# Kernel tuning notes

Hardware: AMD Instinct MI355X
Metric: run time of the kernel (lower is better)

Reference implementation:

```python
import jax, jax.numpy as jnp
import numpy as np

D_MODEL = 1024
NUM_HEADS = 16


def setup_inputs() -> dict:
    key = jax.random.key(0)
    ks = jax.random.split(key, 5)
    std = float(np.sqrt(2.0 / (D_MODEL + D_MODEL)))
    def w(k):
        # approximate trunc_normal init with clipped normal (init only; math of fwd unaffected)
        v = jax.random.truncated_normal(k, -3.0, 3.0, (D_MODEL, D_MODEL), jnp.float32) * std
        return v
    x = jax.random.normal(ks[0], (4, 2048, D_MODEL), jnp.float32)
    return {
        "x": x,
        "wq": w(ks[1]),
        "wk": w(ks[2]),
        "wv": w(ks[3]),
        "wo": w(ks[4]),
    }


def reference(x, wq, wk, wv, wo):
    b, s, d = x.shape
    h = NUM_HEADS
    dk = d // h
    # Linear: einsum('o i, ... i -> ... o')
    def proj(w):
        y = jnp.einsum('oi,bsi->bso', w, x)
        return y.reshape(b, s, h, dk).transpose(0, 2, 1, 3)  # b h s dk
    Q, K, V = proj(wq), proj(wk), proj(wv)
    scale = 1.0 / jnp.sqrt(jnp.asarray(dk, x.dtype))
    scores = jnp.einsum('bhqd,bhkd->bhqk', Q, K) * scale
    mask = jnp.tril(jnp.ones((s, s), dtype=bool))
    scores = jnp.where(mask, scores, -jnp.inf)
    attn = jax.nn.softmax(scores, axis=-1)
    out = jnp.einsum('bhqk,bhkd->bhqd', attn, V)
    out = out.transpose(0, 2, 1, 3).reshape(b, s, d)
    return jnp.einsum('oi,bsi->bso', wo, out)
```

## Files before the change

kernel.cpp:

```cpp
#include <hip/hip_runtime.h>
#include <hip/hip_bf16.h>


typedef __bf16 bf16x8 __attribute__((ext_vector_type(8)));
typedef __bf16 bf16x4 __attribute__((ext_vector_type(4)));
typedef float  f32x4  __attribute__((ext_vector_type(4)));
typedef float  f32x16 __attribute__((ext_vector_type(16)));
typedef unsigned int u32x4_t __attribute__((ext_vector_type(4)));

#define GLOBAL_AS __attribute__((address_space(1)))
#define LDS_AS    __attribute__((address_space(3)))

__device__ __forceinline__ void gload16(const void* g, void* l) {
    __builtin_amdgcn_global_load_lds((const GLOBAL_AS void*)g, (LDS_AS void*)l, 16, 0, 0);
}

__device__ __forceinline__ unsigned int cvtpk_bf16(float lo, float hi) {
    unsigned int r;
    asm("v_cvt_pk_bf16_f32 %0, %1, %2" : "=v"(r) : "v"(lo), "v"(hi));
    return r;
}

#define WAITVM0 asm volatile("s_waitcnt vmcnt(0)" ::: "memory")
#define SCHEDB  __builtin_amdgcn_sched_barrier(0)

__global__ __launch_bounds__(256) void cast_kernel(
    const float* __restrict__ x, const float* __restrict__ wq,
    const float* __restrict__ wk, const float* __restrict__ wv,
    const float* __restrict__ wo, __bf16* __restrict__ xb, __bf16* __restrict__ wb) {
    int bid = blockIdx.x;
    const float* src; __bf16* dst; int base;
    if (bid < 4096) {
        src = x; dst = xb; base = bid * 2048;
    } else {
        int r = bid - 4096; int wi = r >> 9;
        src = (wi == 0) ? wq : (wi == 1) ? wk : (wi == 2) ? wv : wo;
        dst = wb + wi * 1048576; base = (r & 511) * 2048;
    }
    int idx = base + threadIdx.x * 8;
    float4 a = *(const float4*)(src + idx);
    float4 b = *(const float4*)(src + idx + 4);
    bf16x8 o;
    o[0] = (__bf16)a.x; o[1] = (__bf16)a.y; o[2] = (__bf16)a.z; o[3] = (__bf16)a.w;
    o[4] = (__bf16)b.x; o[5] = (__bf16)b.y; o[6] = (__bf16)b.z; o[7] = (__bf16)b.w;
    *(bf16x8*)(dst + idx) = o;
}

__global__ __launch_bounds__(256) void gemm_qkv_kernel(
    const __bf16* __restrict__ A, const __bf16* __restrict__ W,
    __bf16* __restrict__ Qb, __bf16* __restrict__ Kb, __bf16* __restrict__ Vt,
    float qscale) {
    __shared__ __align__(16) char lds[65536];
    const int t = threadIdx.x;
    const int wid = t >> 6, lane = t & 63;
    const int g = lane >> 4, m = lane & 15;
    const int wm = wid >> 1, wn = wid & 1;
    const int bid = (blockIdx.x & 7) * 192 + (blockIdx.x >> 3);
    const int mt = bid / 24, nt = bid % 24;
    const int m0 = mt * 128, n0 = nt * 128;
    const bool isV = (n0 >= 2048);

    const __bf16* sA[4]; const __bf16* sB[4]; int dA[4];
#pragma unroll
    for (int i = 0; i < 4; ++i) {
        const int ci = i * 256 + t;
        const int row = ci >> 3;
        const int k8 = (ci & 7) ^ (row & 7);
        sA[i] = A + (size_t)(m0 + row) * 1024 + k8 * 8;
        sB[i] = W + (size_t)(n0 + row) * 1024 + k8 * 8;
        dA[i] = ci * 16;
    }
    auto stage = [&](int kt, char* buf) {
#pragma unroll
        for (int i = 0; i < 4; ++i) gload16(sA[i] + kt * 64, buf + dA[i]);
#pragma unroll
        for (int i = 0; i < 4; ++i) gload16(sB[i] + kt * 64, buf + 16384 + dA[i]);
    };

    const int sw = (m & 7) << 4;
    const int offA = (wm * 64 + m) * 128 + ((g << 4) ^ sw);
    const int offB = (wn * 64 + m) * 128 + ((g << 4) ^ sw);

    stage(0, lds);

    f32x4 acc[4][4] = {};
    for (int kt = 0; kt < 16; ++kt) {
        char* cbuf = lds + (kt & 1) * 32768;
        WAITVM0;
        SCHEDB;
        __builtin_amdgcn_s_barrier();
        SCHEDB;
        if (kt < 15) stage(kt + 1, lds + ((kt + 1) & 1) * 32768);
        const char* bA = cbuf;
        const char* bB = cbuf + 16384;
        bf16x8 a0[4], b0[4], a1[4], b1[4];
#pragma unroll
        for (int i = 0; i < 4; ++i) {
            a0[i] = *(const bf16x8*)(bA + (offA + i * 2048));
            b0[i] = *(const bf16x8*)(bB + (offB + i * 2048));
            a1[i] = *(const bf16x8*)(bA + ((offA + i * 2048) ^ 64));
            b1[i] = *(const bf16x8*)(bB + ((offB + i * 2048) ^ 64));
        }
        __builtin_amdgcn_s_setprio(1);
        if (isV) {
#pragma unroll
            for (int mi = 0; mi < 4; ++mi)
#pragma unroll
                for (int ni = 0; ni < 4; ++ni)
                    acc[mi][ni] = __builtin_amdgcn_mfma_f32_16x16x32_bf16(a0[mi], b0[ni], acc[mi][ni], 0, 0, 0);
#pragma unroll
            for (int mi = 0; mi < 4; ++mi)
#pragma unroll
                for (int ni = 0; ni < 4; ++ni)
                    acc[mi][ni] = __builtin_amdgcn_mfma_f32_16x16x32_bf16(a1[mi], b1[ni], acc[mi][ni], 0, 0, 0);
        } else {
#pragma unroll
            for (int mi = 0; mi < 4; ++mi)
#pragma unroll
                for (int ni = 0; ni < 4; ++ni)
                    acc[mi][ni] = __builtin_amdgcn_mfma_f32_16x16x32_bf16(b0[ni], a0[mi], acc[mi][ni], 0, 0, 0);
#pragma unroll
            for (int mi = 0; mi < 4; ++mi)
#pragma unroll
                for (int ni = 0; ni < 4; ++ni)
                    acc[mi][ni] = __builtin_amdgcn_mfma_f32_16x16x32_bf16(b1[ni], a1[mi], acc[mi][ni], 0, 0, 0);
        }
        __builtin_amdgcn_s_setprio(0);
    }

    if (isV) {
        const int bb = m0 >> 11;
        const int sb = (m0 & 2047) + wm * 64 + 4 * g;
        const int hbase = ((n0 - 2048) >> 6) + wn;
#pragma unroll
        for (int mi = 0; mi < 4; ++mi)
#pragma unroll
            for (int ni = 0; ni < 4; ++ni) {
                const int d = ni * 16 + m;
                bf16x4 pk;
                pk[0] = (__bf16)(acc[mi][ni][0]); pk[1] = (__bf16)(acc[mi][ni][1]);
                pk[2] = (__bf16)(acc[mi][ni][2]); pk[3] = (__bf16)(acc[mi][ni][3]);
                *(bf16x4*)(Vt + ((size_t)(bb * 16 + hbase) * 64 + d) * 2048 + sb + mi * 16) = pk;
            }
    } else {
        __bf16* C = (n0 < 1024) ? Qb : Kb;
        const float sc = (n0 < 1024) ? qscale : 1.f;
        const int cb = (n0 & 1023) + wn * 64 + 4 * g;
        const int row = m0 + wm * 64 + m;
#pragma unroll
        for (int mi = 0; mi < 4; ++mi)
#pragma unroll
            for (int ni = 0; ni < 4; ++ni) {
                bf16x4 pk;
                pk[0] = (__bf16)(acc[mi][ni][0] * sc); pk[1] = (__bf16)(acc[mi][ni][1] * sc);
                pk[2] = (__bf16)(acc[mi][ni][2] * sc); pk[3] = (__bf16)(acc[mi][ni][3] * sc);
                *(bf16x4*)(C + (size_t)(row + mi * 16) * 1024 + cb + ni * 16) = pk;
            }
    }
}

__global__ __launch_bounds__(256) void gemm_out_kernel(
    const __bf16* __restrict__ A, const __bf16* __restrict__ W, float* __restrict__ out) {
    __shared__ __align__(16) char lds[65536];
    const int t = threadIdx.x;
    const int wid = t >> 6, lane = t & 63;
    const int g = lane >> 4, m = lane & 15;
    const int wm = wid >> 1, wn = wid & 1;
    const int bid = (blockIdx.x & 7) * 64 + (blockIdx.x >> 3);
    const int mt = bid >> 3, nt = bid & 7;
    const int m0 = mt * 128, n0 = nt * 128;

    const __bf16* sA[4]; const __bf16* sB[4]; int dA[4];
#pragma unroll
    for (int i = 0; i < 4; ++i) {
        const int ci = i * 256 + t;
        const int row = ci >> 3;
        const int k8 = (ci & 7) ^ (row & 7);
        sA[i] = A + (size_t)(m0 + row) * 1024 + k8 * 8;
        sB[i] = W + (size_t)(n0 + row) * 1024 + k8 * 8;
        dA[i] = ci * 16;
    }
    auto stage = [&](int kt, char* buf) {
#pragma unroll
        for (int i = 0; i < 4; ++i) gload16(sA[i] + kt * 64, buf + dA[i]);
#pragma unroll
        for (int i = 0; i < 4; ++i) gload16(sB[i] + kt * 64, buf + 16384 + dA[i]);
    };

    const int sw = (m & 7) << 4;
    const int offA = (wm * 64 + m) * 128 + ((g << 4) ^ sw);
    const int offB = (wn * 64 + m) * 128 + ((g << 4) ^ sw);

    stage(0, lds);

    f32x4 acc[4][4] = {};
    for (int kt = 0; kt < 16; ++kt) {
        char* cbuf = lds + (kt & 1) * 32768;
        WAITVM0;
        SCHEDB;
        __builtin_amdgcn_s_barrier();
        SCHEDB;
        if (kt < 15) stage(kt + 1, lds + ((kt + 1) & 1) * 32768);
        const char* bA = cbuf;
        const char* bB = cbuf + 16384;
        bf16x8 a0[4], b0[4], a1[4], b1[4];
#pragma unroll
        for (int i = 0; i < 4; ++i) {
            a0[i] = *(const bf16x8*)(bA + (offA + i * 2048));
            b0[i] = *(const bf16x8*)(bB + (offB + i * 2048));
            a1[i] = *(const bf16x8*)(bA + ((offA + i * 2048) ^ 64));
            b1[i] = *(const bf16x8*)(bB + ((offB + i * 2048) ^ 64));
        }
        __builtin_amdgcn_s_setprio(1);
#pragma unroll
        for (int mi = 0; mi < 4; ++mi)
#pragma unroll
            for (int ni = 0; ni < 4; ++ni)
                acc[mi][ni] = __builtin_amdgcn_mfma_f32_16x16x32_bf16(b0[ni], a0[mi], acc[mi][ni], 0, 0, 0);
#pragma unroll
        for (int mi = 0; mi < 4; ++mi)
#pragma unroll
            for (int ni = 0; ni < 4; ++ni)
                acc[mi][ni] = __builtin_amdgcn_mfma_f32_16x16x32_bf16(b1[ni], a1[mi], acc[mi][ni], 0, 0, 0);
        __builtin_amdgcn_s_setprio(0);
    }

    const int row = m0 + wm * 64 + m;
    const int col = n0 + wn * 64 + 4 * g;
#pragma unroll
    for (int mi = 0; mi < 4; ++mi)
#pragma unroll
        for (int ni = 0; ni < 4; ++ni)
            *(f32x4*)(out + (size_t)(row + mi * 16) * 1024 + col + ni * 16) = acc[mi][ni];
}

__global__ __launch_bounds__(128, 2) void attn_kernel(
    const __bf16* __restrict__ Qb, const __bf16* __restrict__ Kb,
    const __bf16* __restrict__ Vt, __bf16* __restrict__ Ob) {
    __shared__ __align__(16) char lds[32768];
    const int t = threadIdx.x;
    const int w = t >> 6, lane = t & 63;
    const int l31 = lane & 31, hi = lane >> 5;
    const int qb = (blockIdx.x >> 3) & 15;
    const int bh = (blockIdx.x & 7) | ((blockIdx.x >> 7) << 3);
    const size_t sbase = (size_t)(bh >> 4) * 2048;
    const int hoff = (bh & 15) * 64;

    const char* Kbase = (const char*)Kb + (sbase * 1024 + hoff) * 2;
    const char* Vbase = (const char*)Vt + (size_t)bh * 262144;
    const int srow = lane >> 3;
    const int scol = ((lane & 7) ^ srow) << 4;
    const int sw = (l31 & 7) << 4;
    int colx[4];
#pragma unroll
    for (int i = 0; i < 4; ++i) colx[i] = (32 * i + 16 * hi) ^ sw;

    auto stage = [&](int kv0, char* lK) {
        char* lV = lK + 8192;
#pragma unroll
        for (int i = 0; i < 4; ++i) {
            const int chunk = i * 2 + w;
            const int row = chunk * 8 + srow;
            gload16(Kbase + (size_t)(kv0 + row) * 2048 + scol, lK + chunk * 1024);
            gload16(Vbase + (size_t)row * 4096 + (size_t)kv0 * 2 + scol, lV + chunk * 1024);
        }
    };

    const int q0A = qb * 64 + w * 32;
    const int q0B = (31 - qb) * 64 + w * 32;
    const int qA = q0A + l31, qB = q0B + l31;
    const int nstream = 32 - qb;

    const __bf16* qrowA = Qb + (sbase + q0A + l31) * 1024 + hoff + 8 * hi;
    const __bf16* qrowB = Qb + (sbase + q0B + l31) * 1024 + hoff + 8 * hi;
    bf16x8 qfA[4], qfB[4];
#pragma unroll
    for (int cq = 0; cq < 4; ++cq) {
        qfA[cq] = *(const bf16x8*)(qrowA + 16 * cq);
        qfB[cq] = *(const bf16x8*)(qrowB + 16 * cq);
    }

    f32x16 oA0 = {}, oA1 = {}, oB0 = {}, oB1 = {};
    float mA = -__builtin_inff(), lA = 0.f;
    float mB = -__builtin_inff(), lB = 0.f;

    auto process = [&](const f32x16& s0r, const f32x16& s1r, int qq, bool diag,
                       int kv0, float& mrun, float& lrun, f32x16& o0, f32x16& o1,
                       const char* lV) {
        float pp[32];
#pragma unroll
        for (int rr = 0; rr < 16; ++rr) { pp[rr] = s0r[rr]; pp[16 + rr] = s1r[rr]; }
        if (diag) {
#pragma unroll
            for (int rr = 0; rr < 16; ++rr) {
                const int kvl = (rr & 3) + 8 * (rr >> 2) + 4 * hi;
                if (kv0 + kvl > qq)      pp[rr]      = -__builtin_inff();
                if (kv0 + 32 + kvl > qq) pp[16 + rr] = -__builtin_inff();
            }
        }
        float m8[8];
#pragma unroll
        for (int i = 0; i < 8; ++i)
            m8[i] = fmaxf(fmaxf(pp[4 * i], pp[4 * i + 1]), fmaxf(pp[4 * i + 2], pp[4 * i + 3]));
        float tmax = fmaxf(fmaxf(fmaxf(m8[0], m8[1]), fmaxf(m8[2], m8[3])),
                           fmaxf(fmaxf(m8[4], m8[5]), fmaxf(m8[6], m8[7])));
        const bool skip = __all(tmax <= mrun + 8.f);
        if (!skip) {
            float tq = fmaxf(tmax, __shfl_xor(tmax, 32));
            float mnew = fmaxf(mrun, tq);
            float al = __builtin_amdgcn_exp2f(mrun - mnew);
            lrun *= al;
#pragma unroll
            for (int rr = 0; rr < 16; ++rr) { o0[rr] *= al; o1[rr] *= al; }
            mrun = mnew;
        }
#pragma unroll
        for (int rr = 0; rr < 32; ++rr) pp[rr] = __builtin_amdgcn_exp2f(pp[rr] - mrun);
        float s8[8];
#pragma unroll
        for (int i = 0; i < 8; ++i)
            s8[i] = (pp[4 * i] + pp[4 * i + 1]) + (pp[4 * i + 2] + pp[4 * i + 3]);
        float rsum = ((s8[0] + s8[1]) + (s8[2] + s8[3])) + ((s8[4] + s8[5]) + (s8[6] + s8[7]));
        rsum += __shfl_xor(rsum, 32);
        lrun += rsum;

        __builtin_amdgcn_s_setprio(1);
#pragma unroll
        for (int cc = 0; cc < 4; ++cc) {
            const int pb = cc * 8;
            unsigned int A0 = cvtpk_bf16(pp[pb + 0], pp[pb + 1]);
            unsigned int A1 = cvtpk_bf16(pp[pb + 2], pp[pb + 3]);
            unsigned int B0 = cvtpk_bf16(pp[pb + 4], pp[pb + 5]);
            unsigned int B1 = cvtpk_bf16(pp[pb + 6], pp[pb + 7]);
            asm("v_permlane32_swap_b32 %0, %1" : "+v"(A0), "+v"(B0));
            asm("v_permlane32_swap_b32 %0, %1" : "+v"(A1), "+v"(B1));
            u32x4_t wvv; wvv[0] = A0; wvv[1] = A1; wvv[2] = B0; wvv[3] = B1;
            bf16x8 pa = __builtin_bit_cast(bf16x8, wvv);
            const int vcol = (32 * cc + 16 * hi) ^ sw;
            bf16x8 v0 = *(const bf16x8*)(lV + l31 * 128 + vcol);
            bf16x8 v1 = *(const bf16x8*)(lV + (l31 + 32) * 128 + vcol);
            o0 = __builtin_amdgcn_mfma_f32_32x32x16_bf16(v0, pa, o0, 0, 0, 0);
            o1 = __builtin_amdgcn_mfma_f32_32x32x16_bf16(v1, pa, o1, 0, 0, 0);
        }
        __builtin_amdgcn_s_setprio(0);
    };

    stage(0, lds);

    for (int tt = 0; tt < nstream; ++tt) {
        const int cur = tt & 1;
        char* lcur = lds + cur * 16384;
        WAITVM0;
        SCHEDB;
        __builtin_amdgcn_s_barrier();
        SCHEDB;
        if (tt + 1 < nstream) stage((tt + 1) * 64, lds + (cur ^ 1) * 16384);

        const int kv0 = tt * 64;
        const char* lK = lcur;
        const char* lV = lcur + 8192;
        const bool dual = (tt <= qb);

        f32x16 sA0 = {}, sA1 = {}, sB0 = {}, sB1 = {};
        __builtin_amdgcn_s_setprio(1);
        if (dual) {
#pragma unroll
            for (int cc = 0; cc < 4; ++cc) {
                bf16x8 k0 = *(const bf16x8*)(lK + l31 * 128 + colx[cc]);
                bf16x8 k1 = *(const bf16x8*)(lK + (l31 + 32) * 128 + colx[cc]);
                sA0 = __builtin_amdgcn_mfma_f32_32x32x16_bf16(k0, qfA[cc], sA0, 0, 0, 0);
                sA1 = __builtin_amdgcn_mfma_f32_32x32x16_bf16(k1, qfA[cc], sA1, 0, 0, 0);
                sB0 = __builtin_amdgcn_mfma_f32_32x32x16_bf16(k0, qfB[cc], sB0, 0, 0, 0);
                sB1 = __builtin_amdgcn_mfma_f32_32x32x16_bf16(k1, qfB[cc], sB1, 0, 0, 0);
            }
        } else {
#pragma unroll
            for (int cc = 0; cc < 4; ++cc) {
                bf16x8 k0 = *(const bf16x8*)(lK + l31 * 128 + colx[cc]);
                bf16x8 k1 = *(const bf16x8*)(lK + (l31 + 32) * 128 + colx[cc]);
                sB0 = __builtin_amdgcn_mfma_f32_32x32x16_bf16(k0, qfB[cc], sB0, 0, 0, 0);
                sB1 = __builtin_amdgcn_mfma_f32_32x32x16_bf16(k1, qfB[cc], sB1, 0, 0, 0);
            }
        }
        __builtin_amdgcn_s_setprio(0);

        if (dual)
            process(sA0, sA1, qA, tt == qb, kv0, mA, lA, oA0, oA1, lV);
        process(sB0, sB1, qB, tt == nstream - 1, kv0, mB, lB, oB0, oB1, lV);
    }

    {
        const float inv = 1.f / lA;
        __bf16* orow = Ob + (sbase + q0A + l31) * 1024 + hoff;
#pragma unroll
        for (int rq = 0; rq < 4; ++rq) {
            bf16x4 e0, e1;
#pragma unroll
            for (int jj = 0; jj < 4; ++jj) {
                e0[jj] = (__bf16)(oA0[rq * 4 + jj] * inv);
                e1[jj] = (__bf16)(oA1[rq * 4 + jj] * inv);
            }
            *(bf16x4*)(orow + 4 * hi + 8 * rq) = e0;
            *(bf16x4*)(orow + 32 + 4 * hi + 8 * rq) = e1;
        }
    }
    {
        const float inv = 1.f / lB;
        __bf16* orow = Ob + (sbase + q0B + l31) * 1024 + hoff;
#pragma unroll
        for (int rq = 0; rq < 4; ++rq) {
            bf16x4 e0, e1;
#pragma unroll
            for (int jj = 0; jj < 4; ++jj) {
                e0[jj] = (__bf16)(oB0[rq * 4 + jj] * inv);
                e1[jj] = (__bf16)(oB1[rq * 4 + jj] * inv);
            }
            *(bf16x4*)(orow + 4 * hi + 8 * rq) = e0;
            *(bf16x4*)(orow + 32 + 4 * hi + 8 * rq) = e1;
        }
    }
}

extern "C" void kernel_launch(void* const* d_in, const int* in_sizes, int n_in,
                              void* d_out, int out_size, void* d_ws, size_t ws_size,
                              hipStream_t stream) {
    const float* x  = (const float*)d_in[0];
    const float* wq = (const float*)d_in[1];
    const float* wk = (const float*)d_in[2];
    const float* wv = (const float*)d_in[3];
    const float* wo = (const float*)d_in[4];

    char* ws = (char*)d_ws;
    __bf16* xb = (__bf16*)(ws);
    __bf16* wb = (__bf16*)(ws + 16777216);
    __bf16* Qb = (__bf16*)(ws + 25165824);
    __bf16* Kb = (__bf16*)(ws + 41943040);
    __bf16* Vt = (__bf16*)(ws + 58720256);
    __bf16* Ob = (__bf16*)(ws + 75497472);

    const float qscale = 0.18033688011112043f;

    cast_kernel<<<6144, 256, 0, stream>>>(x, wq, wk, wv, wo, xb, wb);
    gemm_qkv_kernel<<<1536, 256, 0, stream>>>(xb, wb, Qb, Kb, Vt, qscale);
    attn_kernel<<<1024, 128, 0, stream>>>(Qb, Kb, Vt, Ob);
    gemm_out_kernel<<<512, 256, 0, stream>>>(Ob, wb + 3145728, (float*)d_out);
}
```

Baseline: 174.3 us.

## Split attention into single-wave blocks with split K/V staging in one buffer

The attention kernel now launches 64-thread single-wave blocks, twice as many as before, and each wave owns its own LDS tile, so the block-wide barrier is gone. K and V are staged into separate halves of a single 16KB buffer. The next K tile is loaded once the score MFMAs have read the current K, and the next V tile once PV has read the current V. Partial vmcnt waits let each load overlap the other half's compute. This removes barriers and double-buffer LDS, which may raise occupancy, but each wave now loads its whole K/V tile alone, doubling global/L2 traffic for K/V compared with the two-wave sharing.

```diff
diff --git a/kernel.cpp b/kernel.cpp
--- a/kernel.cpp
+++ b/kernel.cpp
@@ -21,7 +21,9 @@
     return r;
 }
 
+#define WAITVM8 asm volatile("s_waitcnt vmcnt(8)" ::: "memory")
 #define WAITVM0 asm volatile("s_waitcnt vmcnt(0)" ::: "memory")
+#define WAITLGKM0 asm volatile("s_waitcnt lgkmcnt(0)" ::: "memory")
 #define SCHEDB  __builtin_amdgcn_sched_barrier(0)
 
 __global__ __launch_bounds__(256) void cast_kernel(
@@ -234,15 +236,16 @@
             *(f32x4*)(out + (size_t)(row + mi * 16) * 1024 + col + ni * 16) = acc[mi][ni];
 }
 
-__global__ __launch_bounds__(128, 2) void attn_kernel(
+__global__ __launch_bounds__(64) void attn_kernel(
     const __bf16* __restrict__ Qb, const __bf16* __restrict__ Kb,
     const __bf16* __restrict__ Vt, __bf16* __restrict__ Ob) {
-    __shared__ __align__(16) char lds[32768];
-    const int t = threadIdx.x;
-    const int w = t >> 6, lane = t & 63;
+    __shared__ __align__(16) char lds[16384];
+    const int lane = threadIdx.x & 63;
     const int l31 = lane & 31, hi = lane >> 5;
-    const int qb = (blockIdx.x >> 3) & 15;
-    const int bh = (blockIdx.x & 7) | ((blockIdx.x >> 7) << 3);
+    const int x = blockIdx.x;
+    const int w = (x >> 3) & 1;
+    const int qb = (x >> 4) & 15;
+    const int bh = (x & 7) | ((x >> 8) << 3);
     const size_t sbase = (size_t)(bh >> 4) * 2048;
     const int hoff = (bh & 15) * 64;
 
@@ -255,14 +258,21 @@
 #pragma unroll
     for (int i = 0; i < 4; ++i) colx[i] = (32 * i + 16 * hi) ^ sw;
 
-    auto stage = [&](int kv0, char* lK) {
-        char* lV = lK + 8192;
-#pragma unroll
-        for (int i = 0; i < 4; ++i) {
-            const int chunk = i * 2 + w;
-            const int row = chunk * 8 + srow;
-            gload16(Kbase + (size_t)(kv0 + row) * 2048 + scol, lK + chunk * 1024);
-            gload16(Vbase + (size_t)row * 4096 + (size_t)kv0 * 2 + scol, lV + chunk * 1024);
+    char* lK = lds;
+    char* lV = lds + 8192;
+
+    auto stage_K = [&](int kv0) {
+#pragma unroll
+        for (int i = 0; i < 8; ++i) {
+            const int row = i * 8 + srow;
+            gload16(Kbase + (size_t)(kv0 + row) * 2048 + scol, lK + i * 1024);
+        }
+    };
+    auto stage_V = [&](int kv0) {
+#pragma unroll
+        for (int i = 0; i < 8; ++i) {
+            const int row = i * 8 + srow;
+            gload16(Vbase + (size_t)row * 4096 + (size_t)kv0 * 2 + scol, lV + i * 1024);
         }
     };
 
@@ -285,8 +295,7 @@
     float mB = -__builtin_inff(), lB = 0.f;
 
     auto process = [&](const f32x16& s0r, const f32x16& s1r, int qq, bool diag,
-                       int kv0, float& mrun, float& lrun, f32x16& o0, f32x16& o1,
-                       const char* lV) {
+                       int kv0, float& mrun, float& lrun, f32x16& o0, f32x16& o1) {
         float pp[32];
 #pragma unroll
         for (int rr = 0; rr < 16; ++rr) { pp[rr] = s0r[rr]; pp[16 + rr] = s1r[rr]; }
@@ -345,20 +354,15 @@
         __builtin_amdgcn_s_setprio(0);
     };
 
-    stage(0, lds);
+    stage_K(0);
+    stage_V(0);
 
     for (int tt = 0; tt < nstream; ++tt) {
-        const int cur = tt & 1;
-        char* lcur = lds + cur * 16384;
-        WAITVM0;
-        SCHEDB;
-        __builtin_amdgcn_s_barrier();
-        SCHEDB;
-        if (tt + 1 < nstream) stage((tt + 1) * 64, lds + (cur ^ 1) * 16384);
+        const bool last = (tt + 1 == nstream);
+        WAITVM8;
+        SCHEDB;
 
         const int kv0 = tt * 64;
-        const char* lK = lcur;
-        const char* lV = lcur + 8192;
         const bool dual = (tt <= qb);
 
         f32x16 sA0 = {}, sA1 = {}, sB0 = {}, sB1 = {};
@@ -383,10 +387,20 @@
             }
         }
         __builtin_amdgcn_s_setprio(0);
+        WAITLGKM0;
+        SCHEDB;
+        if (!last) stage_K(kv0 + 64);
+
+        if (!last) { WAITVM8; } else { WAITVM0; }
+        SCHEDB;
 
         if (dual)
-            process(sA0, sA1, qA, tt == qb, kv0, mA, lA, oA0, oA1, lV);
-        process(sB0, sB1, qB, tt == nstream - 1, kv0, mB, lB, oB0, oB1, lV);
+            process(sA0, sA1, qA, tt == qb, kv0, mA, lA, oA0, oA1);
+        process(sB0, sB1, qB, last, kv0, mB, lB, oB0, oB1);
+
+        WAITLGKM0;
+        SCHEDB;
+        if (!last) stage_V(kv0 + 64);
     }
 
     {
@@ -442,6 +456,6 @@
 
     cast_kernel<<<6144, 256, 0, stream>>>(x, wq, wk, wv, wo, xb, wb);
     gemm_qkv_kernel<<<1536, 256, 0, stream>>>(xb, wb, Qb, Kb, Vt, qscale);
-    attn_kernel<<<1024, 128, 0, stream>>>(Qb, Kb, Vt, Ob);
+    attn_kernel<<<2048, 64, 0, stream>>>(Qb, Kb, Vt, Ob);
     gemm_out_kernel<<<512, 256, 0, stream>>>(Ob, wb + 3145728, (float*)d_out);
 }
```

Result: slower. 215.4 us (+23.6%).

## Enlarge QKV GEMM tiles to 256x256 with 8 waves and phased prefetch

Applied to the files above, without the earlier changes.

The QKV projection GEMM moves from 128x128 tiles with 4 waves to 256x256 tiles with 8 waves, using 128KB of LDS and 384 blocks. The K loop is split into four quadrant phases, each issuing part of the next tiles' global-to-LDS loads, with partial vmcnt waits and barriers between phases. The goal is more operand reuse per byte loaded and better overlap of loads with MFMA work. In exchange there are more barriers per k-step, fewer blocks (384 for 256 CUs, so a tail wave), and higher register and LDS pressure.

```diff
diff --git a/kernel.cpp b/kernel.cpp
--- a/kernel.cpp
+++ b/kernel.cpp
@@ -21,7 +21,10 @@
     return r;
 }
 
+#define WAITVM8 asm volatile("s_waitcnt vmcnt(8)" ::: "memory")
+#define WAITVM6 asm volatile("s_waitcnt vmcnt(6)" ::: "memory")
 #define WAITVM0 asm volatile("s_waitcnt vmcnt(0)" ::: "memory")
+#define WAITLGKM0 asm volatile("s_waitcnt lgkmcnt(0)" ::: "memory")
 #define SCHEDB  __builtin_amdgcn_sched_barrier(0)
 
 __global__ __launch_bounds__(256) void cast_kernel(
@@ -46,94 +49,137 @@
     *(bf16x8*)(dst + idx) = o;
 }
 
-__global__ __launch_bounds__(256) void gemm_qkv_kernel(
+__global__ __launch_bounds__(512) void gemm_qkv_kernel(
     const __bf16* __restrict__ A, const __bf16* __restrict__ W,
     __bf16* __restrict__ Qb, __bf16* __restrict__ Kb, __bf16* __restrict__ Vt,
     float qscale) {
-    __shared__ __align__(16) char lds[65536];
+    __shared__ __align__(16) char lds[131072];
     const int t = threadIdx.x;
     const int wid = t >> 6, lane = t & 63;
     const int g = lane >> 4, m = lane & 15;
-    const int wm = wid >> 1, wn = wid & 1;
-    const int bid = (blockIdx.x & 7) * 192 + (blockIdx.x >> 3);
-    const int mt = bid / 24, nt = bid % 24;
-    const int m0 = mt * 128, n0 = nt * 128;
+    const int wm = wid >> 2, wn = wid & 3;
+    const int bid = (blockIdx.x & 7) * 48 + (blockIdx.x >> 3);
+    const int mt = bid / 12, nt = bid % 12;
+    const int m0 = mt * 256, n0 = nt * 256;
     const bool isV = (n0 >= 2048);
 
-    const __bf16* sA[4]; const __bf16* sB[4]; int dA[4];
-#pragma unroll
-    for (int i = 0; i < 4; ++i) {
-        const int ci = i * 256 + t;
-        const int row = ci >> 3;
-        const int k8 = (ci & 7) ^ (row & 7);
-        sA[i] = A + (size_t)(m0 + row) * 1024 + k8 * 8;
-        sB[i] = W + (size_t)(n0 + row) * 1024 + k8 * 8;
-        dA[i] = ci * 16;
-    }
-    auto stage = [&](int kt, char* buf) {
-#pragma unroll
-        for (int i = 0; i < 4; ++i) gload16(sA[i] + kt * 64, buf + dA[i]);
-#pragma unroll
-        for (int i = 0; i < 4; ++i) gload16(sB[i] + kt * 64, buf + 16384 + dA[i]);
+    const __bf16* aSrc[2][2]; int aDst[2][2];
+    const __bf16* bSrc[2][2]; int bDst[2][2];
+#pragma unroll
+    for (int q = 0; q < 2; ++q) {
+        const int j = t + q * 512;
+        const int slot = j & 7;
+        {
+            const int r0 = (j >> 9) * 128 + ((j >> 3) & 63);
+            aSrc[0][q] = A + (size_t)(m0 + r0) * 1024 + (slot ^ (r0 & 7)) * 8;
+            aDst[0][q] = r0 * 128 + slot * 16;
+            const int r1 = r0 + 64;
+            aSrc[1][q] = A + (size_t)(m0 + r1) * 1024 + (slot ^ (r1 & 7)) * 8;
+            aDst[1][q] = r1 * 128 + slot * 16;
+        }
+        {
+            const int r0 = ((j >> 8) & 3) * 64 + ((j >> 3) & 31);
+            bSrc[0][q] = W + (size_t)(n0 + r0) * 1024 + (slot ^ (r0 & 7)) * 8;
+            bDst[0][q] = r0 * 128 + slot * 16;
+            const int r1 = r0 + 32;
+            bSrc[1][q] = W + (size_t)(n0 + r1) * 1024 + (slot ^ (r1 & 7)) * 8;
+            bDst[1][q] = r1 * 128 + slot * 16;
+        }
+    }
+    auto stageA = [&](int par, int kt, int d) {
+        gload16(aSrc[par][0] + kt * 64, lds + d * 65536 + aDst[par][0]);
+        gload16(aSrc[par][1] + kt * 64, lds + d * 65536 + aDst[par][1]);
     };
+    auto stageB = [&](int par, int kt, int d) {
+        gload16(bSrc[par][0] + kt * 64, lds + d * 65536 + 32768 + bDst[par][0]);
+        gload16(bSrc[par][1] + kt * 64, lds + d * 65536 + 32768 + bDst[par][1]);
+    };
 
     const int sw = (m & 7) << 4;
-    const int offA = (wm * 64 + m) * 128 + ((g << 4) ^ sw);
-    const int offB = (wn * 64 + m) * 128 + ((g << 4) ^ sw);
-
-    stage(0, lds);
-
-    f32x4 acc[4][4] = {};
+    const int offA0 = (wm * 128 + m) * 128 + ((g << 4) ^ sw);
+    const int offB0 = (wn * 64 + m) * 128 + ((g << 4) ^ sw);
+
+    stageA(0, 0, 0); stageA(1, 0, 0); stageB(0, 0, 0); stageB(1, 0, 0);
+    stageA(0, 1, 1); stageB(0, 1, 1);
+    WAITVM6;
+    SCHEDB;
+    __builtin_amdgcn_s_barrier();
+    SCHEDB;
+
+    f32x4 acc[8][4] = {};
+
+#define QPHASE(MH, NH, WVM, ...)                                              \
+    {                                                                         \
+        const char* bA_ = lds + bufd * 65536;                                 \
+        const char* bB_ = bA_ + 32768;                                        \
+        bf16x8 af[4][2], bfr[2][2];                                           \
+        _Pragma("unroll")                                                     \
+        for (int i2 = 0; i2 < 4; ++i2) {                                      \
+            const int off = offA0 + ((MH) * 4 + i2) * 2048;                   \
+            af[i2][0] = *(const bf16x8*)(bA_ + off);                          \
+            af[i2][1] = *(const bf16x8*)(bA_ + (off ^ 64));                   \
+        }                                                                     \
+        _Pragma("unroll")                                                     \
+        for (int j2 = 0; j2 < 2; ++j2) {                                      \
+            const int off = offB0 + ((NH) * 2 + j2) * 2048;                   \
+            bfr[j2][0] = *(const bf16x8*)(bB_ + off);                         \
+            bfr[j2][1] = *(const bf16x8*)(bB_ + (off ^ 64));                  \
+        }                                                                     \
+        __VA_ARGS__;                                                          \
+        WVM; SCHEDB;                                                          \
+        __builtin_amdgcn_s_barrier();                                         \
+        WAITLGKM0; SCHEDB;                                                    \
+        __builtin_amdgcn_s_setprio(1);                                        \
+        if (isV) {                                                            \
+            _Pragma("unroll")                                                 \
+            for (int i2 = 0; i2 < 4; ++i2)                                    \
+                _Pragma("unroll")                                             \
+                for (int j2 = 0; j2 < 2; ++j2) {                              \
+                    acc[(MH)*4+i2][(NH)*2+j2] = __builtin_amdgcn_mfma_f32_16x16x32_bf16( \
+                        af[i2][0], bfr[j2][0], acc[(MH)*4+i2][(NH)*2+j2], 0, 0, 0);      \
+                    acc[(MH)*4+i2][(NH)*2+j2] = __builtin_amdgcn_mfma_f32_16x16x32_bf16( \
+                        af[i2][1], bfr[j2][1], acc[(MH)*4+i2][(NH)*2+j2], 0, 0, 0);      \
+                }                                                             \
+        } else {                                                              \
+            _Pragma("unroll")                                                 \
+            for (int i2 = 0; i2 < 4; ++i2)                                    \
+                _Pragma("unroll")                                             \
+                for (int j2 = 0; j2 < 2; ++j2) {                              \
+                    acc[(MH)*4+i2][(NH)*2+j2] = __builtin_amdgcn_mfma_f32_16x16x32_bf16( \
+                        bfr[j2][0], af[i2][0], acc[(MH)*4+i2][(NH)*2+j2], 0, 0, 0);      \
+                    acc[(MH)*4+i2][(NH)*2+j2] = __builtin_amdgcn_mfma_f32_16x16x32_bf16( \
+                        bfr[j2][1], af[i2][1], acc[(MH)*4+i2][(NH)*2+j2], 0, 0, 0);      \
+                }                                                             \
+        }                                                                     \
+        __builtin_amdgcn_s_setprio(0);                                        \
+        SCHEDB;                                                               \
+        __builtin_amdgcn_s_barrier();                                         \
+        SCHEDB;                                                               \
+    }
+
     for (int kt = 0; kt < 16; ++kt) {
-        char* cbuf = lds + (kt & 1) * 32768;
-        WAITVM0;
-        SCHEDB;
-        __builtin_amdgcn_s_barrier();
-        SCHEDB;
-        if (kt < 15) stage(kt + 1, lds + ((kt + 1) & 1) * 32768);
-        const char* bA = cbuf;
-        const char* bB = cbuf + 16384;
-        bf16x8 a0[4], b0[4], a1[4], b1[4];
-#pragma unroll
-        for (int i = 0; i < 4; ++i) {
-            a0[i] = *(const bf16x8*)(bA + (offA + i * 2048));
-            b0[i] = *(const bf16x8*)(bB + (offB + i * 2048));
-            a1[i] = *(const bf16x8*)(bA + ((offA + i * 2048) ^ 64));
-            b1[i] = *(const bf16x8*)(bB + ((offB + i * 2048) ^ 64));
-        }
-        __builtin_amdgcn_s_setprio(1);
-        if (isV) {
-#pragma unroll
-            for (int mi = 0; mi < 4; ++mi)
-#pragma unroll
-                for (int ni = 0; ni < 4; ++ni)
-                    acc[mi][ni] = __builtin_amdgcn_mfma_f32_16x16x32_bf16(a0[mi], b0[ni], acc[mi][ni], 0, 0, 0);
-#pragma unroll
-            for (int mi = 0; mi < 4; ++mi)
-#pragma unroll
-                for (int ni = 0; ni < 4; ++ni)
-                    acc[mi][ni] = __builtin_amdgcn_mfma_f32_16x16x32_bf16(a1[mi], b1[ni], acc[mi][ni], 0, 0, 0);
+        const int bufd = kt & 1;
+        const int nb = bufd ^ 1;
+        if (kt < 15) {
+            QPHASE(0, 0, WAITVM6, if (kt + 1 < 16) stageA(1, kt + 1, nb));
+            QPHASE(0, 1, WAITVM6, if (kt + 1 < 16) stageB(1, kt + 1, nb));
+            QPHASE(1, 0, WAITVM6, if (kt + 2 < 16) stageA(0, kt + 2, bufd));
+            QPHASE(1, 1, WAITVM6, if (kt + 2 < 16) stageB(0, kt + 2, bufd));
         } else {
-#pragma unroll
-            for (int mi = 0; mi < 4; ++mi)
-#pragma unroll
-                for (int ni = 0; ni < 4; ++ni)
-                    acc[mi][ni] = __builtin_amdgcn_mfma_f32_16x16x32_bf16(b0[ni], a0[mi], acc[mi][ni], 0, 0, 0);
-#pragma unroll
-            for (int mi = 0; mi < 4; ++mi)
-#pragma unroll
-                for (int ni = 0; ni < 4; ++ni)
-                    acc[mi][ni] = __builtin_amdgcn_mfma_f32_16x16x32_bf16(b1[ni], a1[mi], acc[mi][ni], 0, 0, 0);
-        }
-        __builtin_amdgcn_s_setprio(0);
-    }
+            QPHASE(0, 0, WAITVM0, );
+            QPHASE(0, 1, WAITVM0, );
+            QPHASE(1, 0, WAITVM0, );
+            QPHASE(1, 1, WAITVM0, );
+        }
+    }
+#undef QPHASE
 
     if (isV) {
         const int bb = m0 >> 11;
-        const int sb = (m0 & 2047) + wm * 64 + 4 * g;
+        const int sb = (m0 & 2047) + wm * 128 + 4 * g;
         const int hbase = ((n0 - 2048) >> 6) + wn;
 #pragma unroll
-        for (int mi = 0; mi < 4; ++mi)
+        for (int mi = 0; mi < 8; ++mi)
 #pragma unroll
             for (int ni = 0; ni < 4; ++ni) {
                 const int d = ni * 16 + m;
@@ -146,9 +192,9 @@
         __bf16* C = (n0 < 1024) ? Qb : Kb;
         const float sc = (n0 < 1024) ? qscale : 1.f;
         const int cb = (n0 & 1023) + wn * 64 + 4 * g;
-        const int row = m0 + wm * 64 + m;
-#pragma unroll
-        for (int mi = 0; mi < 4; ++mi)
+        const int row = m0 + wm * 128 + m;
+#pragma unroll
+        for (int mi = 0; mi < 8; ++mi)
 #pragma unroll
             for (int ni = 0; ni < 4; ++ni) {
                 bf16x4 pk;
@@ -441,7 +487,7 @@
     const float qscale = 0.18033688011112043f;
 
     cast_kernel<<<6144, 256, 0, stream>>>(x, wq, wk, wv, wo, xb, wb);
-    gemm_qkv_kernel<<<1536, 256, 0, stream>>>(xb, wb, Qb, Kb, Vt, qscale);
+    gemm_qkv_kernel<<<384, 512, 0, stream>>>(xb, wb, Qb, Kb, Vt, qscale);
     attn_kernel<<<1024, 128, 0, stream>>>(Qb, Kb, Vt, Ob);
     gemm_out_kernel<<<512, 256, 0, stream>>>(Ob, wb + 3145728, (float*)d_out);
 }
```

New measurement: 194.3 us. +11.4%, slower.
